# Kernel tuning notes

Measured on AMD Instinct MI355X. Metric: run time of the kernel, lower is better.

## Reference

```python
import jax, jax.numpy as jnp
import numpy as np

J, E = 17, 4096
LN_EPS = 1e-5

BONE_PAIRS = np.array([[0,1],[1,2],[2,3],[0,4],[4,5],[5,6],[0,7],[7,8],[8,9],[9,10],
                       [8,11],[11,12],[12,13],[8,14],[14,15],[15,16]], dtype=np.int32)

def _xavier(key, fan_in, fan_out, gain=0.5):
    limit = gain * np.sqrt(6.0 / (fan_in + fan_out))
    return jax.random.uniform(key, (fan_in, fan_out), jnp.float32, -limit, limit)

def setup_inputs() -> dict:
    key = jax.random.key(0)
    k0, k1, k2 = jax.random.split(key, 3)
    return {
        "joint_embeddings": jax.random.normal(k0, (J, E), jnp.float32) * 0.02,
        "W1": _xavier(k1, 2 * E, E),
        "b1": jnp.zeros((E,), jnp.float32),
        "g1": jnp.ones((E,), jnp.float32),
        "be1": jnp.zeros((E,), jnp.float32),
        "W2": _xavier(k2, E, E),
        "b2": jnp.zeros((E,), jnp.float32),
        "g2": jnp.ones((E,), jnp.float32),
        "be2": jnp.zeros((E,), jnp.float32),
        "bone_pairs": jnp.asarray(BONE_PAIRS),
    }

def _layernorm(x, g, b):
    mu = jnp.mean(x, axis=-1, keepdims=True)
    var = jnp.mean(jnp.square(x - mu), axis=-1, keepdims=True)
    return (x - mu) * jax.lax.rsqrt(var + LN_EPS) * g + b

def reference(joint_embeddings, W1, b1, g1, be1, W2, b2, g2, be2, bone_pairs):
    # L2-normalize each joint embedding (torch F.normalize, eps=1e-12), scale by sqrt(E)
    norm = jnp.linalg.norm(joint_embeddings, axis=-1, keepdims=True)
    joint_emb = joint_embeddings / jnp.maximum(norm, 1e-12)
    joint_emb = joint_emb * jnp.sqrt(jnp.float32(E))
    # gather both endpoints of each bone, concat -> [16, 2E]
    pair_emb = jnp.concatenate([joint_emb[bone_pairs[:, 0]], joint_emb[bone_pairs[:, 1]]], axis=-1)
    # 2-layer MLP with LayerNorm; Dropout(0.1) is identity in eval
    h = jax.nn.relu(_layernorm(pair_emb @ W1 + b1, g1, be1))
    bone_features = _layernorm(h @ W2 + b2, g2, be2)
    return (joint_emb, bone_features)
```

## Files before the change

kernel.cpp:

```cpp
#include <hip/hip_runtime.h>
#include <math.h>

#define J 17
#define E 4096
#define M 16
#define LN_EPS 1e-5f

__global__ void norm17_kernel(const float* __restrict__ je, float* __restrict__ out) {
    const int row = blockIdx.x;
    const float* __restrict__ src = je + (size_t)row * E;
    float* __restrict__ dst = out + (size_t)row * E;

    float ss = 0.0f;
    float4 v[4];
    #pragma unroll
    for (int i = 0; i < 4; ++i) {
        int idx = threadIdx.x + i * 256;
        v[i] = ((const float4*)src)[idx];
        ss += v[i].x * v[i].x + v[i].y * v[i].y + v[i].z * v[i].z + v[i].w * v[i].w;
    }
    for (int off = 32; off; off >>= 1) ss += __shfl_down(ss, off, 64);
    __shared__ float red[4];
    if ((threadIdx.x & 63) == 0) red[threadIdx.x >> 6] = ss;
    __syncthreads();
    float total = red[0] + red[1] + red[2] + red[3];

    float scale = 64.0f / fmaxf(sqrtf(total), 1e-12f);
    #pragma unroll
    for (int i = 0; i < 4; ++i) {
        int idx = threadIdx.x + i * 256;
        float4 o = v[i];
        o.x *= scale; o.y *= scale; o.z *= scale; o.w *= scale;
        ((float4*)dst)[idx] = o;
    }
}

template <int KTOT, int KC, bool GATHER>
__global__ __launch_bounds__(256) void skinny_gemm_kernel(
        const float* __restrict__ X,
        const float* __restrict__ W,
        float* __restrict__ out,
        const int* __restrict__ pairs,
        const float* __restrict__ joint) {

    __shared__ float xs[M][KC];
    const int k0 = blockIdx.x * KC;

    for (int s = threadIdx.x; s < M * KC / 4; s += 256) {
        const int m  = s / (KC / 4);
        const int k4 = s % (KC / 4);
        const float* srow;
        if (GATHER) {
            const int half = (k0 >= E) ? 1 : 0;
            const int j = pairs[2 * m + half];
            srow = joint + (size_t)j * E + (k0 & (E - 1));
        } else {
            srow = X + (size_t)m * KTOT + k0;
        }
        ((float4*)&xs[m][0])[k4] = ((const float4*)srow)[k4];
    }
    __syncthreads();

    const int col = blockIdx.y * 512 + threadIdx.x * 2;
    float2 acc[M];
    #pragma unroll
    for (int m = 0; m < M; ++m) { acc[m].x = 0.0f; acc[m].y = 0.0f; }

    const float* __restrict__ wp = W + (size_t)k0 * E + col;
    #pragma unroll 4
    for (int k = 0; k < KC; ++k) {
        const float2 w = *(const float2*)wp;
        wp += E;
        #pragma unroll
        for (int m = 0; m < M; ++m) {
            const float xv = xs[m][k];
            acc[m].x = fmaf(xv, w.x, acc[m].x);
            acc[m].y = fmaf(xv, w.y, acc[m].y);
        }
    }

    #pragma unroll
    for (int m = 0; m < M; ++m) {
        atomicAdd(&out[(size_t)m * E + col],     acc[m].x);
        atomicAdd(&out[(size_t)m * E + col + 1], acc[m].y);
    }
}

__global__ void ln_row_kernel(const float* __restrict__ pre,
                              const float* __restrict__ bias,
                              const float* __restrict__ g,
                              const float* __restrict__ be,
                              float* __restrict__ out,
                              int relu) {
    const int r = blockIdx.x;
    const float* __restrict__ src = pre + (size_t)r * E;

    float4 v[4];
    float s = 0.0f, s2 = 0.0f;
    #pragma unroll
    for (int i = 0; i < 4; ++i) {
        int idx = threadIdx.x + i * 256;
        float4 p = ((const float4*)src)[idx];
        float4 b = ((const float4*)bias)[idx];
        p.x += b.x; p.y += b.y; p.z += b.z; p.w += b.w;
        v[i] = p;
        s  += p.x + p.y + p.z + p.w;
        s2 += p.x * p.x + p.y * p.y + p.z * p.z + p.w * p.w;
    }
    for (int off = 32; off; off >>= 1) {
        s  += __shfl_down(s,  off, 64);
        s2 += __shfl_down(s2, off, 64);
    }
    __shared__ float ra[4], rb[4];
    if ((threadIdx.x & 63) == 0) { ra[threadIdx.x >> 6] = s; rb[threadIdx.x >> 6] = s2; }
    __syncthreads();
    s  = ra[0] + ra[1] + ra[2] + ra[3];
    s2 = rb[0] + rb[1] + rb[2] + rb[3];

    const float mu  = s * (1.0f / E);
    const float var = s2 * (1.0f / E) - mu * mu;
    const float rs  = rsqrtf(var + LN_EPS);

    #pragma unroll
    for (int i = 0; i < 4; ++i) {
        int idx = threadIdx.x + i * 256;
        float4 gg = ((const float4*)g)[idx];
        float4 bb = ((const float4*)be)[idx];
        float4 o;
        o.x = (v[i].x - mu) * rs * gg.x + bb.x;
        o.y = (v[i].y - mu) * rs * gg.y + bb.y;
        o.z = (v[i].z - mu) * rs * gg.z + bb.z;
        o.w = (v[i].w - mu) * rs * gg.w + bb.w;
        if (relu) {
            o.x = fmaxf(o.x, 0.0f); o.y = fmaxf(o.y, 0.0f);
            o.z = fmaxf(o.z, 0.0f); o.w = fmaxf(o.w, 0.0f);
        }
        ((float4*)(out + (size_t)r * E))[idx] = o;
    }
}

extern "C" void kernel_launch(void* const* d_in, const int* in_sizes, int n_in,
                              void* d_out, int out_size, void* d_ws, size_t ws_size,
                              hipStream_t stream) {
    const float* je  = (const float*)d_in[0];
    const float* W1  = (const float*)d_in[1];
    const float* b1  = (const float*)d_in[2];
    const float* g1  = (const float*)d_in[3];
    const float* be1 = (const float*)d_in[4];
    const float* W2  = (const float*)d_in[5];
    const float* b2  = (const float*)d_in[6];
    const float* g2  = (const float*)d_in[7];
    const float* be2 = (const float*)d_in[8];
    const int*   bp  = (const int*)d_in[9];

    float* out       = (float*)d_out;
    float* joint_out = out;
    float* bone_out  = out + J * E;

    float* pre1 = (float*)d_ws;
    float* pre2 = pre1 + M * E;
    float* h    = pre2 + M * E;

    hipMemsetAsync(d_ws, 0, 2 * (size_t)M * E * sizeof(float), stream);

    norm17_kernel<<<J, 256, 0, stream>>>(je, joint_out);

    skinny_gemm_kernel<2 * E, 128, true><<<dim3(64, 8), 256, 0, stream>>>(
        nullptr, W1, pre1, bp, joint_out);

    ln_row_kernel<<<M, 256, 0, stream>>>(pre1, b1, g1, be1, h, 1);

    skinny_gemm_kernel<E, 128, false><<<dim3(32, 8), 256, 0, stream>>>(
        h, W2, pre2, nullptr, nullptr);

    ln_row_kernel<<<M, 256, 0, stream>>>(pre2, b2, g2, be2, bone_out, 0);
}
```

Before: 313.0 us.

## Widen GEMM tiles to float4, prefetch weights, replace atomics with partial-sum reduction

```diff
diff --git a/kernel.cpp b/kernel.cpp
--- a/kernel.cpp
+++ b/kernel.cpp
@@ -35,11 +35,35 @@
     }
 }
 
-template <int KTOT, int KC, bool GATHER>
-__global__ __launch_bounds__(256) void skinny_gemm_kernel(
+#define DO_GROUP(KB, W0, W1, W2, W3)                                  \
+    {                                                                 \
+        _Pragma("unroll")                                             \
+        for (int m = 0; m < M; ++m) {                                 \
+            const float4 xv = *(const float4*)&xs[m][(KB)];           \
+            acc[m].x = fmaf(xv.x, W0.x, acc[m].x);                    \
+            acc[m].x = fmaf(xv.y, W1.x, acc[m].x);                    \
+            acc[m].x = fmaf(xv.z, W2.x, acc[m].x);                    \
+            acc[m].x = fmaf(xv.w, W3.x, acc[m].x);                    \
+            acc[m].y = fmaf(xv.x, W0.y, acc[m].y);                    \
+            acc[m].y = fmaf(xv.y, W1.y, acc[m].y);                    \
+            acc[m].y = fmaf(xv.z, W2.y, acc[m].y);                    \
+            acc[m].y = fmaf(xv.w, W3.y, acc[m].y);                    \
+            acc[m].z = fmaf(xv.x, W0.z, acc[m].z);                    \
+            acc[m].z = fmaf(xv.y, W1.z, acc[m].z);                    \
+            acc[m].z = fmaf(xv.z, W2.z, acc[m].z);                    \
+            acc[m].z = fmaf(xv.w, W3.z, acc[m].z);                    \
+            acc[m].w = fmaf(xv.x, W0.w, acc[m].w);                    \
+            acc[m].w = fmaf(xv.y, W1.w, acc[m].w);                    \
+            acc[m].w = fmaf(xv.z, W2.w, acc[m].w);                    \
+            acc[m].w = fmaf(xv.w, W3.w, acc[m].w);                    \
+        }                                                             \
+    }
+
+template <int KTOT, int KC, bool GATHER, bool PARTIAL>
+__global__ __launch_bounds__(256) void gemm_kernel(
         const float* __restrict__ X,
         const float* __restrict__ W,
-        float* __restrict__ out,
+        float* __restrict__ part,
         const int* __restrict__ pairs,
         const float* __restrict__ joint) {
 
@@ -52,8 +76,7 @@
         const float* srow;
         if (GATHER) {
             const int half = (k0 >= E) ? 1 : 0;
-            const int j = pairs[2 * m + half];
-            srow = joint + (size_t)j * E + (k0 & (E - 1));
+            srow = joint + (size_t)pairs[2 * m + half] * E + (k0 & (E - 1));
         } else {
             srow = X + (size_t)m * KTOT + k0;
         }
@@ -61,29 +84,79 @@
     }
     __syncthreads();
 
-    const int col = blockIdx.y * 512 + threadIdx.x * 2;
-    float2 acc[M];
-    #pragma unroll
-    for (int m = 0; m < M; ++m) { acc[m].x = 0.0f; acc[m].y = 0.0f; }
-
+    const int col = blockIdx.y * 1024 + (threadIdx.x << 2);
     const float* __restrict__ wp = W + (size_t)k0 * E + col;
-    #pragma unroll 4
-    for (int k = 0; k < KC; ++k) {
-        const float2 w = *(const float2*)wp;
-        wp += E;
+
+    float4 acc[M];
+    #pragma unroll
+    for (int m = 0; m < M; ++m) acc[m] = make_float4(0.f, 0.f, 0.f, 0.f);
+
+    float4 wa0 = *(const float4*)(wp + (size_t)0 * E);
+    float4 wa1 = *(const float4*)(wp + (size_t)1 * E);
+    float4 wa2 = *(const float4*)(wp + (size_t)2 * E);
+    float4 wa3 = *(const float4*)(wp + (size_t)3 * E);
+    float4 wb0 = *(const float4*)(wp + (size_t)4 * E);
+    float4 wb1 = *(const float4*)(wp + (size_t)5 * E);
+    float4 wb2 = *(const float4*)(wp + (size_t)6 * E);
+    float4 wb3 = *(const float4*)(wp + (size_t)7 * E);
+
+    int kk = 0;
+    for (; kk + 8 < KC; kk += 8) {
+        DO_GROUP(kk, wa0, wa1, wa2, wa3);
+        wa0 = *(const float4*)(wp + (size_t)(kk + 8)  * E);
+        wa1 = *(const float4*)(wp + (size_t)(kk + 9)  * E);
+        wa2 = *(const float4*)(wp + (size_t)(kk + 10) * E);
+        wa3 = *(const float4*)(wp + (size_t)(kk + 11) * E);
+        DO_GROUP(kk + 4, wb0, wb1, wb2, wb3);
+        wb0 = *(const float4*)(wp + (size_t)(kk + 12) * E);
+        wb1 = *(const float4*)(wp + (size_t)(kk + 13) * E);
+        wb2 = *(const float4*)(wp + (size_t)(kk + 14) * E);
+        wb3 = *(const float4*)(wp + (size_t)(kk + 15) * E);
+    }
+    DO_GROUP(kk,     wa0, wa1, wa2, wa3);
+    DO_GROUP(kk + 4, wb0, wb1, wb2, wb3);
+
+    if (PARTIAL) {
+        float* dst = part + ((size_t)blockIdx.x * M) * E + col;
         #pragma unroll
         for (int m = 0; m < M; ++m) {
-            const float xv = xs[m][k];
-            acc[m].x = fmaf(xv, w.x, acc[m].x);
-            acc[m].y = fmaf(xv, w.y, acc[m].y);
-        }
-    }
-
-    #pragma unroll
-    for (int m = 0; m < M; ++m) {
-        atomicAdd(&out[(size_t)m * E + col],     acc[m].x);
-        atomicAdd(&out[(size_t)m * E + col + 1], acc[m].y);
-    }
+            *(float4*)(dst + (size_t)m * E) = acc[m];
+        }
+    } else {
+        #pragma unroll
+        for (int m = 0; m < M; ++m) {
+            atomicAdd(&part[(size_t)m * E + col + 0], acc[m].x);
+            atomicAdd(&part[(size_t)m * E + col + 1], acc[m].y);
+            atomicAdd(&part[(size_t)m * E + col + 2], acc[m].z);
+            atomicAdd(&part[(size_t)m * E + col + 3], acc[m].w);
+        }
+    }
+}
+
+template <int CHUNKS>
+__global__ __launch_bounds__(64) void reduce_kernel(const float* __restrict__ part,
+                                                    float* __restrict__ pre) {
+    const size_t f = ((size_t)blockIdx.x * 64 + threadIdx.x) * 4;
+    const float* p = part + f;
+    float4 s0 = make_float4(0.f, 0.f, 0.f, 0.f);
+    float4 s1 = s0, s2 = s0, s3 = s0;
+    #pragma unroll
+    for (int c = 0; c < CHUNKS; c += 4) {
+        const float4 a = *(const float4*)(p + (size_t)(c + 0) * (M * E));
+        const float4 b = *(const float4*)(p + (size_t)(c + 1) * (M * E));
+        const float4 d = *(const float4*)(p + (size_t)(c + 2) * (M * E));
+        const float4 e = *(const float4*)(p + (size_t)(c + 3) * (M * E));
+        s0.x += a.x; s0.y += a.y; s0.z += a.z; s0.w += a.w;
+        s1.x += b.x; s1.y += b.y; s1.z += b.z; s1.w += b.w;
+        s2.x += d.x; s2.y += d.y; s2.z += d.z; s2.w += d.w;
+        s3.x += e.x; s3.y += e.y; s3.z += e.z; s3.w += e.w;
+    }
+    float4 o;
+    o.x = (s0.x + s1.x) + (s2.x + s3.x);
+    o.y = (s0.y + s1.y) + (s2.y + s3.y);
+    o.z = (s0.z + s1.z) + (s2.z + s3.z);
+    o.w = (s0.w + s1.w) + (s2.w + s3.w);
+    *(float4*)(pre + f) = o;
 }
 
 __global__ void ln_row_kernel(const float* __restrict__ pre,
@@ -157,21 +230,37 @@
     float* joint_out = out;
     float* bone_out  = out + J * E;
 
-    float* pre1 = (float*)d_ws;
-    float* pre2 = pre1 + M * E;
-    float* h    = pre2 + M * E;
-
-    hipMemsetAsync(d_ws, 0, 2 * (size_t)M * E * sizeof(float), stream);
+    const size_t part_floats = (size_t)64 * M * E;
+    const size_t need = (part_floats + 3 * (size_t)M * E) * sizeof(float);
 
     norm17_kernel<<<J, 256, 0, stream>>>(je, joint_out);
 
-    skinny_gemm_kernel<2 * E, 128, true><<<dim3(64, 8), 256, 0, stream>>>(
-        nullptr, W1, pre1, bp, joint_out);
-
-    ln_row_kernel<<<M, 256, 0, stream>>>(pre1, b1, g1, be1, h, 1);
-
-    skinny_gemm_kernel<E, 128, false><<<dim3(32, 8), 256, 0, stream>>>(
-        h, W2, pre2, nullptr, nullptr);
-
-    ln_row_kernel<<<M, 256, 0, stream>>>(pre2, b2, g2, be2, bone_out, 0);
-}
+    if (ws_size >= need) {
+        float* part = (float*)d_ws;
+        float* pre1 = part + part_floats;
+        float* pre2 = pre1 + (size_t)M * E;
+        float* h    = pre2 + (size_t)M * E;
+
+        gemm_kernel<2 * E, 128, true, true><<<dim3(64, 4), 256, 0, stream>>>(
+            nullptr, W1, part, bp, joint_out);
+        reduce_kernel<64><<<256, 64, 0, stream>>>(part, pre1);
+        ln_row_kernel<<<M, 256, 0, stream>>>(pre1, b1, g1, be1, h, 1);
+
+        gemm_kernel<E, 64, false, true><<<dim3(64, 4), 256, 0, stream>>>(
+            h, W2, part, nullptr, nullptr);
+        reduce_kernel<64><<<256, 64, 0, stream>>>(part, pre2);
+        ln_row_kernel<<<M, 256, 0, stream>>>(pre2, b2, g2, be2, bone_out, 0);
+    } else {
+        float* pre1 = (float*)d_ws;
+        float* pre2 = pre1 + (size_t)M * E;
+        float* h    = pre2 + (size_t)M * E;
+        hipMemsetAsync(d_ws, 0, 2 * (size_t)M * E * sizeof(float), stream);
+
+        gemm_kernel<2 * E, 128, true, false><<<dim3(64, 4), 256, 0, stream>>>(
+            nullptr, W1, pre1, bp, joint_out);
+        ln_row_kernel<<<M, 256, 0, stream>>>(pre1, b1, g1, be1, h, 1);
+        gemm_kernel<E, 64, false, false><<<dim3(64, 4), 256, 0, stream>>>(
+            h, W2, pre2, nullptr, nullptr);
+        ln_row_kernel<<<M, 256, 0, stream>>>(pre2, b2, g2, be2, bone_out, 0);
+    }
+}
```

Result: faster. 277.8 us (-11.3%).
